# Performance work log

Hardware: AMD Instinct MI355X
Metric: run time of the kernel (lower is better)

Reference implementation:

```python
import jax, jax.numpy as jnp
import numpy as np

C = 256      # in_channels
H = 16       # num_heads
K = 7        # tconv kernel size
P1 = 8       # type_1 partition size
P2 = 8       # type_2 partition size
HB = H // 4  # heads per attention branch (= 4)
EPS = 1e-5


def _ln(x, g, b):
    m = x.mean(-1, keepdims=True)
    v = ((x - m) ** 2).mean(-1, keepdims=True)
    return (x - m) / jnp.sqrt(v + EPS) * g + b


def _window_attn(parts, table, heads, P):
    # parts: [B_, P, 3*Cb]; table: [2P-1, heads]
    B_, N, _ = parts.shape
    qkv = parts.reshape(B_, N, 3, heads, -1).transpose(2, 0, 3, 1, 4)  # [3,B_,h,P,d]
    q, k, v = qkv[0], qkv[1], qkv[2]
    scale = heads ** (-0.5)  # NOTE: module scales by num_heads**-0.5 (faithful)
    attn = jnp.einsum('bhnd,bhmd->bhnm', q * scale, k)
    idx = (jnp.arange(P)[:, None] - jnp.arange(P)[None, :]) + P - 1  # [P,P]
    bias = table[idx].transpose(2, 0, 1)  # [h,P,P]
    attn = jax.nn.softmax(attn + bias[None], axis=-1)
    out = jnp.einsum('bhnm,bhmd->bhnd', attn, v)
    return out.transpose(0, 2, 1, 3).reshape(B_, N, -1)


def _type1_part(x, P):  # x: [B,Cc,T] contiguous windows
    B, Cc, T = x.shape
    return x.reshape(B, Cc, T // P, P).transpose(0, 2, 3, 1).reshape(-1, P, Cc)


def _type1_rev(y, B, Cc, T, P):
    return y.reshape(B, T // P, P, Cc).transpose(0, 3, 1, 2).reshape(B, Cc, T)


def _type2_part(x, P):  # strided (dilated) windows
    B, Cc, T = x.shape
    return x.reshape(B, Cc, P, T // P).transpose(0, 3, 2, 1).reshape(-1, P, Cc)


def _type2_rev(y, B, Cc, T, P):
    return y.reshape(B, T // P, P, Cc).transpose(0, 3, 2, 1).reshape(B, Cc, T)


def setup_inputs() -> dict:
    key = jax.random.key(0)
    ks = jax.random.split(key, 16)
    B, T = 16, 8192
    d = {
        'x': jax.random.normal(ks[0], (B, C, T), jnp.float32),
        'g1': jnp.ones((C,), jnp.float32),
        'b1': jnp.zeros((C,), jnp.float32),
        'Wm': jax.random.normal(ks[1], (C, 2 * C), jnp.float32) * 0.02,
        'bm': jnp.zeros((2 * C,), jnp.float32),
        'Wc': jax.random.normal(ks[2], (C // 2, (C // 2) // (H // 2), K), jnp.float32) * 0.05,
        'bc': jnp.zeros((C // 2,), jnp.float32),
        'tab1': jax.random.normal(ks[3], (2 * P1 - 1, HB), jnp.float32) * 0.02,
        'tab2': jax.random.normal(ks[4], (2 * P2 - 1, HB), jnp.float32) * 0.02,
        'Wp': jax.random.normal(ks[5], (C, C), jnp.float32) * 0.02,
        'bp': jnp.zeros((C,), jnp.float32),
        'g2': jnp.ones((C,), jnp.float32),
        'b2': jnp.zeros((C,), jnp.float32),
        'W1': jax.random.normal(ks[6], (C, 4 * C), jnp.float32) * 0.02,
        'bf1': jnp.zeros((4 * C,), jnp.float32),
        'W2': jax.random.normal(ks[7], (4 * C, C), jnp.float32) * 0.02,
        'bf2': jnp.zeros((C,), jnp.float32),
    }
    return d


def _forward(x, g1, b1, Wm, bm, Wc, bc, tab1, tab2, Wp, bp, g2, b2, W1, bf1, W2, bf2):
    B, Cin, T = x.shape
    xt = x.transpose(0, 2, 1)  # [B,T,C]
    skip = xt
    f = (_ln(xt, g1, b1) @ Wm + bm).transpose(0, 2, 1)  # [B,2C,T]
    f_conv, f_attn = f[:, :Cin // 2], f[:, Cin // 2:]
    # grouped temporal conv, padding SAME
    y0 = jax.lax.conv_general_dilated(
        f_conv, Wc, window_strides=(1,), padding=[((K - 1) // 2, (K - 1) // 2)],
        feature_group_count=H // 2, dimension_numbers=('NCH', 'OIH', 'NCH')) + bc[None, :, None]
    Cb3 = 3 * Cin // 4
    fa1, fa2 = f_attn[:, :Cb3], f_attn[:, Cb3:]
    y1 = _type1_rev(_window_attn(_type1_part(fa1, P1), tab1, HB, P1), B, Cin // 4, T, P1)
    y2 = _type2_rev(_window_attn(_type2_part(fa2, P2), tab2, HB, P2), B, Cin // 4, T, P2)
    out = jnp.concatenate([y0, y1, y2], axis=1).transpose(0, 2, 1) @ Wp + bp
    out = skip + out
    h = _ln(out, g2, b2)
    h = jax.nn.gelu(h @ W1 + bf1, approximate=False) @ W2 + bf2
    out = out + h
    return out.transpose(0, 2, 1)  # [B,C,T]


def reference(x, g1, b1, Wm, bm, Wc, bc, tab1, tab2, Wp, bp, g2, b2, W1, bf1, W2, bf2):
    return _forward(x, g1, b1, Wm, bm, Wc, bc, tab1, tab2, Wp, bp, g2, b2, W1, bf1, W2, bf2)
```

## Files before the change

kernel.cpp:

```cpp
#include <hip/hip_runtime.h>
#include <hip/hip_bf16.h>

#define DI __device__ __forceinline__

typedef unsigned short u16;
typedef __attribute__((ext_vector_type(4))) float f32x4;
typedef __attribute__((ext_vector_type(8))) short short8;
typedef __attribute__((ext_vector_type(4))) short short4v;

constexpr int Bb = 16, Tt = 8192;
constexpr int M_TOT = Bb * Tt;

static DI u16 f2bf(float f) {
    union { float f; unsigned u; } v; v.f = f;
    unsigned r = v.u + 0x7fffu + ((v.u >> 16) & 1u);
    return (u16)(r >> 16);
}
static DI float bf2f(u16 u) {
    union { unsigned u; float f; } v; v.u = ((unsigned)u) << 16;
    return v.f;
}
static DI float bf2f_s(short s) { return bf2f((u16)s); }

static DI void lds_load16(const void* g, void* l) {
    __builtin_amdgcn_global_load_lds(
        (const __attribute__((address_space(1))) void*)g,
        (__attribute__((address_space(3))) void*)l, 16, 0, 0);
}

static DI float gelu_fast(float x) {
    float x2 = x * x;
    float z2 = x * (2.30220723f + 0.10294515f * x2);
    float e;
    asm("v_exp_f32 %0, %1" : "=v"(e) : "v"(z2));
    float r = __builtin_amdgcn_rcpf(1.f + e);
    return x - x * r;
}

__global__ void prep_weights(const float* __restrict__ Wm, const float* __restrict__ Wp,
                             const float* __restrict__ W1, const float* __restrict__ W2,
                             const float* __restrict__ Wc,
                             const float* __restrict__ g1, const float* __restrict__ b1,
                             const float* __restrict__ g2, const float* __restrict__ b2,
                             const float* __restrict__ bm, const float* __restrict__ bf1,
                             u16* __restrict__ WmT, u16* __restrict__ WpT,
                             u16* __restrict__ W1T, u16* __restrict__ W2T,
                             u16* __restrict__ WtC,
                             float* __restrict__ bmF, float* __restrict__ b1F) {
    int i = blockIdx.x * blockDim.x + threadIdx.x;
    int stride = gridDim.x * blockDim.x;
    for (int j = i; j < 512 * 256; j += stride) {
        int n = j >> 8, k = j & 255;
        WmT[j] = f2bf(Wm[k * 512 + n] * g1[k]);
    }
    for (int j = i; j < 256 * 256; j += stride) {
        int n = j >> 8, k = j & 255;
        WpT[j] = f2bf(Wp[k * 256 + n]);
    }
    for (int j = i; j < 1024 * 256; j += stride) {
        int n = j >> 8, k = j & 255;
        W1T[j] = f2bf(W1[k * 1024 + n] * g2[k]);
    }
    for (int j = i; j < 256 * 1024; j += stride) {
        int n = j >> 10, k = j & 1023;
        W2T[j] = f2bf(W2[k * 256 + n]);
    }
    for (int j = i; j < 128 * 128; j += stride) {
        int co = j >> 7, kp = j & 127;
        int tap = kp >> 4, ci = kp & 15;
        float v = (tap < 7) ? Wc[(co * 16 + ci) * 7 + tap] : 0.f;
        WtC[j] = f2bf(v);
    }
    for (int n = i; n < 512; n += stride) {
        float s = bm[n];
        for (int k = 0; k < 256; ++k) s += b1[k] * Wm[k * 512 + n];
        bmF[n] = s;
    }
    for (int n = i; n < 1024; n += stride) {
        float s = bf1[n];
        for (int k = 0; k < 256; ++k) s += b2[k] * W1[k * 1024 + n];
        b1F[n] = s;
    }
}

__global__ __launch_bounds__(256) void ln1_kernel(const float* __restrict__ x,
                                                  u16* __restrict__ xln,
                                                  u16* __restrict__ xt) {
    __shared__ u16 tile[64 * 256];
    __shared__ float ps[64 * 16], pss[64 * 16];
    __shared__ float smean[64], srstd[64];
    int bidx = blockIdx.x;
    int b = bidx >> 7;
    int t0 = (bidx & 127) << 6;
    int tid = threadIdx.x, l = tid & 63, w = tid >> 6;
    int lr = l & 15, lg = l >> 4;
    float s[4] = {}, ss[4] = {};
    #pragma unroll 4
    for (int it = 0; it < 16; ++it) {
        int c = it * 16 + w * 4 + lg;
        f32x4 v = *(const f32x4*)&x[((size_t)b * 256 + c) * 8192 + t0 + lr * 4];
        #pragma unroll
        for (int k = 0; k < 4; ++k) {
            s[k] += v[k]; ss[k] += v[k] * v[k];
            int t = lr * 4 + k;
            int c8 = c >> 3;
            int slot = (c8 & 24) | ((c8 ^ t) & 7);
            tile[t * 256 + slot * 8 + (c & 7)] = f2bf(v[k]);
        }
    }
    #pragma unroll
    for (int k = 0; k < 4; ++k) {
        ps[(lr * 4 + k) * 16 + w * 4 + lg] = s[k];
        pss[(lr * 4 + k) * 16 + w * 4 + lg] = ss[k];
    }
    __syncthreads();
    if (tid < 64) {
        float sum = 0.f, sq = 0.f;
        #pragma unroll
        for (int g = 0; g < 16; ++g) { sum += ps[tid * 16 + g]; sq += pss[tid * 16 + g]; }
        float m = sum * (1.f / 256.f);
        smean[tid] = m;
        srstd[tid] = rsqrtf(sq * (1.f / 256.f) - m * m + 1e-5f);
    }
    __syncthreads();
    int r = tid >> 2, q = tid & 3;
    float m = smean[r], rs = srstd[r];
    size_t rowbase = ((size_t)b * 8192 + t0 + r) * 256;
    #pragma unroll
    for (int u = 0; u < 8; ++u) {
        int c0 = q * 64 + u * 8;
        int c8 = c0 >> 3;
        int slot = (c8 & 24) | ((c8 ^ r) & 7);
        short8 d = *(const short8*)&tile[r * 256 + slot * 8];
        *(short8*)&xt[rowbase + c0] = d;
        short8 o;
        #pragma unroll
        for (int j = 0; j < 8; ++j)
            o[j] = (short)f2bf((bf2f_s(d[j]) - m) * rs);
        *(short8*)&xln[rowbase + c0] = o;
    }
}

template<int EPI, int N, int K>
__global__ __launch_bounds__(256) void gemm_bt2(const u16* __restrict__ A,
                                                const u16* __restrict__ Bt,
                                                const float* __restrict__ bias,
                                                u16* __restrict__ outb,
                                                const u16* __restrict__ skipx) {
    constexpr int NB = N / 128;
    int bid = blockIdx.x;
    int x8 = bid & 7;
    int rest = bid >> 3;
    int ni = rest % NB;
    int mi = (rest / NB) * 8 + x8;
    int m0 = mi * 128, n0 = ni * 128;
    __shared__ u16 As[2][128 * 64];
    __shared__ u16 Bs[2][128 * 64];
    int tid = threadIdx.x, l = tid & 63, w = tid >> 6;
    int mrow = (w >> 1) * 64, ncol = (w & 1) * 64;
    int lr = l & 15, lg = l >> 4;
    f32x4 acc[4][4] = {};
    auto stage = [&](int buf, int k0) {
        #pragma unroll
        for (int p = 0; p < 4; ++p) {
            int cb = p * 256 + w * 64;
            int chunk = cb + l;
            int row = chunk >> 3, k8 = chunk & 7;
            int k8s = k8 ^ (row & 7);
            lds_load16(A  + (size_t)(m0 + row) * K + k0 + k8s * 8, &As[buf][cb * 8]);
            lds_load16(Bt + (size_t)(n0 + row) * K + k0 + k8s * 8, &Bs[buf][cb * 8]);
        }
    };
    stage(0, 0);
    __syncthreads();
    constexpr int NT = K / 64;
    int buf = 0;
    for (int t = 0; t < NT; ++t) {
        if (t + 1 < NT) stage(buf ^ 1, (t + 1) * 64);
        __builtin_amdgcn_s_setprio(1);
        #pragma unroll
        for (int kk = 0; kk < 64; kk += 32) {
            short8 a[4], bfr[4];
            #pragma unroll
            for (int i = 0; i < 4; ++i) {
                int r = mrow + i * 16 + lr;
                a[i] = *(const short8*)&As[buf][r * 64 + ((((kk >> 3) + lg) ^ (r & 7)) << 3)];
            }
            #pragma unroll
            for (int j = 0; j < 4; ++j) {
                int r = ncol + j * 16 + lr;
                bfr[j] = *(const short8*)&Bs[buf][r * 64 + ((((kk >> 3) + lg) ^ (r & 7)) << 3)];
            }
            #pragma unroll
            for (int i = 0; i < 4; ++i)
                #pragma unroll
                for (int j = 0; j < 4; ++j)
                    acc[i][j] = __builtin_amdgcn_mfma_f32_16x16x32_bf16(a[i], bfr[j], acc[i][j], 0, 0, 0);
        }
        __builtin_amdgcn_s_setprio(0);
        __syncthreads();
        buf ^= 1;
    }
    #pragma unroll
    for (int i = 0; i < 4; ++i) {
        int row0 = m0 + mrow + i * 16 + lg * 4;
        #pragma unroll
        for (int j = 0; j < 4; ++j) {
            int col = n0 + ncol + j * 16 + lr;
            float bv = bias[col];
            f32x4 v = acc[i][j];
            if constexpr (EPI == 0) {
                #pragma unroll
                for (int r = 0; r < 4; ++r)
                    outb[(size_t)(row0 + r) * N + col] = f2bf(v[r] + bv);
            } else {
                #pragma unroll
                for (int r = 0; r < 4; ++r)
                    outb[(size_t)(row0 + r) * N + col] =
                        f2bf(v[r] + bv + bf2f(skipx[(size_t)(row0 + r) * 256 + col]));
            }
        }
    }
}

__global__ __launch_bounds__(1024, 1) void ffn_fused7(const u16* __restrict__ outb,
                                                      const u16* __restrict__ W1g,
                                                      const float* __restrict__ b1F,
                                                      const u16* __restrict__ W2T,
                                                      const float* __restrict__ bf2v,
                                                      float* __restrict__ out) {
    __shared__ u16 W1c[2][64 * 256];
    __shared__ u16 W2c[2][256 * 64];
    __shared__ u16 hbuf[128 * 64];
    int bid = blockIdx.x;
    int m0 = bid * 128;
    int tid = threadIdx.x, l = tid & 63, w = tid >> 6;
    int lr = l & 15, lg = l >> 4;
    int wm1 = w >> 1, wn1 = w & 1;
    int wm2 = w >> 2, wn2 = w & 3;

    short8 a_reg[8];
    {
        size_t base = (size_t)(m0 + wm1 * 16 + lr) * 256 + lg * 8;
        float s = 0.f, ss = 0.f;
        #pragma unroll
        for (int ks = 0; ks < 8; ++ks) {
            short8 rv = *(const short8*)&outb[base + ks * 32];
            a_reg[ks] = rv;
            #pragma unroll
            for (int e = 0; e < 8; ++e) { float v = bf2f_s(rv[e]); s += v; ss += v * v; }
        }
        s += __shfl_xor(s, 16); ss += __shfl_xor(ss, 16);
        s += __shfl_xor(s, 32); ss += __shfl_xor(ss, 32);
        float m = s * (1.f / 256.f);
        float rs = rsqrtf(ss * (1.f / 256.f) - m * m + 1e-5f);
        #pragma unroll
        for (int ks = 0; ks < 8; ++ks) {
            short8 rv = a_reg[ks], ov;
            #pragma unroll
            for (int e = 0; e < 8; ++e) ov[e] = (short)f2bf((bf2f_s(rv[e]) - m) * rs);
            a_reg[ks] = ov;
        }
    }

    auto stageW1 = [&](int buf, int c) {
        #pragma unroll
        for (int p = 0; p < 2; ++p) {
            int cb = p * 1024 + w * 64;
            int chunk = cb + l;
            int row = chunk >> 5, sl = chunk & 31;
            int sl2 = (sl & 24) | ((sl ^ row) & 7);
            lds_load16(W1g + (size_t)(c * 64 + row) * 256 + sl2 * 8, &W1c[buf][cb * 8]);
        }
    };
    auto stageW2 = [&](int buf, int c) {
        #pragma unroll
        for (int p = 0; p < 2; ++p) {
            int cb = p * 1024 + w * 64;
            int chunk = cb + l;
            int row = chunk >> 3, sl = chunk & 7;
            int sl2 = sl ^ (row & 7);
            lds_load16(W2T + (size_t)row * 1024 + c * 64 + sl2 * 8, &W2c[buf][cb * 8]);
        }
    };
    stageW1(0, 0); stageW2(0, 0);
    f32x4 acc2[2][4] = {};
    __syncthreads();

    for (int c = 0; c < 16; ++c) {
        int buf = c & 1;
        f32x4 acc1[2] = {};
        __builtin_amdgcn_s_setprio(1);
        #pragma unroll
        for (int ks = 0; ks < 8; ++ks) {
            short8 wf[2];
            #pragma unroll
            for (int nt = 0; nt < 2; ++nt) {
                int n = wn1 * 32 + nt * 16 + lr;
                int sl = ks * 4 + lg;
                int sl2 = (sl & 24) | ((sl ^ n) & 7);
                wf[nt] = *(const short8*)&W1c[buf][n * 256 + sl2 * 8];
            }
            #pragma unroll
            for (int nt = 0; nt < 2; ++nt)
                acc1[nt] = __builtin_amdgcn_mfma_f32_16x16x32_bf16(
                    wf[nt], a_reg[ks], acc1[nt], 0, 0, 0);
        }
        __builtin_amdgcn_s_setprio(0);
        if (c < 15) { stageW1(buf ^ 1, c + 1); stageW2(buf ^ 1, c + 1); }
        #pragma unroll
        for (int nt = 0; nt < 2; ++nt) {
            int colb = wn1 * 32 + nt * 16 + lg * 4;
            int row = wm1 * 16 + lr;
            f32x4 bv4 = *(const f32x4*)&b1F[c * 64 + colb];
            float g0 = gelu_fast(acc1[nt][0] + bv4[0]);
            float g1v = gelu_fast(acc1[nt][1] + bv4[1]);
            float g2v = gelu_fast(acc1[nt][2] + bv4[2]);
            float g3v = gelu_fast(acc1[nt][3] + bv4[3]);
            uint2 dd;
            asm("v_cvt_pk_bf16_f32 %0, %1, %2" : "=v"(dd.x) : "v"(g0), "v"(g1v));
            asm("v_cvt_pk_bf16_f32 %0, %1, %2" : "=v"(dd.y) : "v"(g2v), "v"(g3v));
            int sl2 = (colb >> 3) ^ (row & 7);
            *(uint2*)&hbuf[row * 64 + sl2 * 8 + (colb & 7)] = dd;
        }
        asm volatile("s_waitcnt lgkmcnt(0)" ::: "memory");
        __builtin_amdgcn_s_barrier();
        __builtin_amdgcn_sched_barrier(0);
        __builtin_amdgcn_s_setprio(1);
        #pragma unroll
        for (int ks = 0; ks < 2; ++ks) {
            short8 hf[2], w2f[4];
            #pragma unroll
            for (int mt = 0; mt < 2; ++mt) {
                int row = wm2 * 32 + mt * 16 + lr;
                int sl2 = (ks * 4 + lg) ^ (row & 7);
                hf[mt] = *(const short8*)&hbuf[row * 64 + sl2 * 8];
            }
            #pragma unroll
            for (int nt = 0; nt < 4; ++nt) {
                int n = wn2 * 64 + nt * 16 + lr;
                int sl2 = (ks * 4 + lg) ^ (n & 7);
                w2f[nt] = *(const short8*)&W2c[buf][n * 64 + sl2 * 8];
            }
            #pragma unroll
            for (int mt = 0; mt < 2; ++mt)
                #pragma unroll
                for (int nt = 0; nt < 4; ++nt)
                    acc2[mt][nt] = __builtin_amdgcn_mfma_f32_16x16x32_bf16(
                        hf[mt], w2f[nt], acc2[mt][nt], 0, 0, 0);
        }
        __builtin_amdgcn_s_setprio(0);
        __syncthreads();
    }
    int bb_ = m0 >> 13;
    int tb = m0 & 8191;
    #pragma unroll
    for (int mt = 0; mt < 2; ++mt) {
        int row0 = wm2 * 32 + mt * 16 + lg * 4;
        #pragma unroll
        for (int nt = 0; nt < 4; ++nt) {
            int col = wn2 * 64 + nt * 16 + lr;
            float bv = bf2v[col];
            f32x4 o;
            #pragma unroll
            for (int r = 0; r < 4; ++r)
                o[r] = acc2[mt][nt][r] + bv + bf2f(outb[(size_t)(m0 + row0 + r) * 256 + col]);
            *(f32x4*)&out[((size_t)bb_ * 256 + col) * 8192 + tb + row0] = o;
        }
    }
}

__global__ __launch_bounds__(256) void mixer_kernel(const u16* __restrict__ f,
                                                    const u16* __restrict__ WtC,
                                                    const float* __restrict__ bc,
                                                    const float* __restrict__ tab1,
                                                    const float* __restrict__ tab2,
                                                    u16* __restrict__ att) {
    __shared__ u16 smem[25600];
    __shared__ float stab[60];
    int bid = blockIdx.x;
    int path = bid % 3;
    int inner = bid / 3;
    int b = inner >> 7;
    int tid = threadIdx.x, l = tid & 63, w = tid >> 6;

    if (path == 0) {
        u16* fs = smem;
        u16* wt = smem + 9216;
        int t0 = (inner & 127) << 6;
        #pragma unroll
        for (int k = 0; k < 8; ++k) {
            int c = tid + k * 256;
            int row = c >> 4, sl = c & 15;
            int c8s = (sl & 8) | ((sl ^ row) & 7);
            lds_load16(WtC + row * 128 + c8s * 8, &wt[(w * 64 + (tid & 63)) * 8 + k * 256 * 8]);
        }
        for (int c = tid; c < 72 * 16; c += 256) {
            int rrow = c >> 4, c8 = c & 15;
            int t = t0 - 3 + rrow;
            uint4 v = {0u, 0u, 0u, 0u};
            if (t >= 0 && t < 8192)
                v = *(const uint4*)&f[((size_t)b * 8192 + t) * 512 + c8 * 8];
            int slot = (c8 & 8) | ((c8 ^ rrow) & 7);
            *(uint4*)&fs[rrow * 128 + slot * 8] = v;
        }
        __syncthreads();
        int wr = w >> 1, wc = w & 1;
        int lr = l & 15, lg = l >> 4;
        f32x4 acc[2][4] = {};
        #pragma unroll
        for (int kk = 0; kk < 4; ++kk) {
            int kp = kk * 32 + lg * 8;
            int tap = kp >> 4, ci = kp & 15;
            #pragma unroll
            for (int i = 0; i < 2; ++i) {
                int trow = wr * 32 + i * 16 + lr;
                #pragma unroll
                for (int g = 0; g < 4; ++g) {
                    int ra = trow + tap;
                    int ea = (wc * 4 + g) * 2 + (ci >> 3);
                    short8 a = *(const short8*)&fs[ra * 128 + (((ea & 8) | ((ea ^ ra) & 7)) << 3)];
                    int nb = (wc * 4 + g) * 16 + lr;
                    int eb = kp >> 3;
                    short8 bfr = *(const short8*)&wt[nb * 128 + (((eb & 8) | ((eb ^ nb) & 7)) << 3)];
                    acc[i][g] = __builtin_amdgcn_mfma_f32_16x16x32_bf16(a, bfr, acc[i][g], 0, 0, 0);
                }
            }
        }
        #pragma unroll
        for (int i = 0; i < 2; ++i) {
            int trow = wr * 32 + i * 16 + lg * 4;
            #pragma unroll
            for (int g = 0; g < 4; ++g) {
                int co = (wc * 4 + g) * 16 + lr;
                float bv = bc[co];
                #pragma unroll
                for (int r = 0; r < 4; ++r) {
                    int t = t0 + trow + r;
                    att[((size_t)b * 8192 + t) * 256 + co] = f2bf(acc[i][g][r] + bv);
                }
            }
        }
    } else {
        u16* qkv = smem;
        const int QBASE = (path == 1) ? 128 : 320;
        const int OBASE = (path == 1) ? 128 : 192;
        const float* tab = (path == 1) ? tab1 : tab2;
        int j0 = (inner & 127) << 3;
        if (tid < 60) stab[tid] = tab[tid];
        for (int c = tid; c < 64 * 24; c += 256) {
            int ridx = c / 24, off = (c % 24) << 3;
            int wl = ridx >> 3, n = ridx & 7;
            int t = (path == 1) ? ((j0 + wl) * 8 + n) : (n * 1024 + j0 + wl);
            *(uint4*)&qkv[ridx * 200 + off] = *(const uint4*)&f[((size_t)b * 8192 + t) * 512 + QBASE + off];
        }
        __syncthreads();
        int wl = tid >> 5, h = (tid >> 3) & 3, n = tid & 7;
        const u16* qr = &qkv[(wl * 8 + n) * 200 + h * 16];
        float q[16];
        {
            short8 q0 = *(const short8*)qr, q1 = *(const short8*)(qr + 8);
            #pragma unroll
            for (int d = 0; d < 8; ++d) { q[d] = bf2f_s(q0[d]); q[d + 8] = bf2f_s(q1[d]); }
        }
        float s[8];
        #pragma unroll
        for (int m = 0; m < 8; ++m) {
            const u16* kr = &qkv[(wl * 8 + m) * 200 + 64 + h * 16];
            short8 k0 = *(const short8*)kr, k1 = *(const short8*)(kr + 8);
            float a = 0.f;
            #pragma unroll
            for (int d = 0; d < 8; ++d) a += q[d] * bf2f_s(k0[d]) + q[d + 8] * bf2f_s(k1[d]);
            s[m] = 0.5f * a + stab[(n - m + 7) * 4 + h];
        }
        float mx = s[0];
        #pragma unroll
        for (int m = 1; m < 8; ++m) mx = fmaxf(mx, s[m]);
        float sum = 0.f;
        #pragma unroll
        for (int m = 0; m < 8; ++m) { s[m] = __expf(s[m] - mx); sum += s[m]; }
        float rinv = 1.f / sum;
        float o[16] = {};
        #pragma unroll
        for (int m = 0; m < 8; ++m) {
            float p = s[m] * rinv;
            const u16* vr = &qkv[(wl * 8 + m) * 200 + 128 + h * 16];
            short8 v0 = *(const short8*)vr, v1 = *(const short8*)(vr + 8);
            #pragma unroll
            for (int d = 0; d < 8; ++d) { o[d] += p * bf2f_s(v0[d]); o[d + 8] += p * bf2f_s(v1[d]); }
        }
        int t = (path == 1) ? ((j0 + wl) * 8 + n) : (n * 1024 + j0 + wl);
        short8 o0, o1;
        #pragma unroll
        for (int d = 0; d < 8; ++d) { o0[d] = (short)f2bf(o[d]); o1[d] = (short)f2bf(o[d + 8]); }
        u16* op = &att[((size_t)b * 8192 + t) * 256 + OBASE + h * 16];
        *(short8*)op = o0; *(short8*)(op + 8) = o1;
    }
}

extern "C" void kernel_launch(void* const* d_in, const int* in_sizes, int n_in,
                              void* d_out, int out_size, void* d_ws, size_t ws_size,
                              hipStream_t stream) {
    const float* x    = (const float*)d_in[0];
    const float* g1   = (const float*)d_in[1];
    const float* b1   = (const float*)d_in[2];
    const float* Wm   = (const float*)d_in[3];
    const float* bm   = (const float*)d_in[4];
    const float* Wc   = (const float*)d_in[5];
    const float* bc   = (const float*)d_in[6];
    const float* tab1 = (const float*)d_in[7];
    const float* tab2 = (const float*)d_in[8];
    const float* Wp   = (const float*)d_in[9];
    const float* bp   = (const float*)d_in[10];
    const float* g2   = (const float*)d_in[11];
    const float* b2   = (const float*)d_in[12];
    const float* W1   = (const float*)d_in[13];
    const float* bf1  = (const float*)d_in[14];
    const float* W2   = (const float*)d_in[15];
    const float* bf2  = (const float*)d_in[16];
    float* out = (float*)d_out;

    char* ws = (char*)d_ws;
    u16* f    = (u16*)(ws);
    u16* att  = (u16*)(ws + 134217728);
    u16* outb = (u16*)(ws + 201326592);
    u16* xlnb = (u16*)(ws + 268435456);
    u16* xt   = (u16*)(ws + 335544320);
    char* wb = ws + 402653184;
    u16* WmT   = (u16*)wb;
    u16* WpT   = (u16*)(wb + 262144);
    u16* W1T   = (u16*)(wb + 393216);
    u16* W2T   = (u16*)(wb + 917504);
    u16* WtC   = (u16*)(wb + 1441792);
    float* bmF = (float*)(wb + 1474560);
    float* b1F = (float*)(wb + 1476608);

    prep_weights<<<512, 256, 0, stream>>>(Wm, Wp, W1, W2, Wc, g1, b1, g2, b2, bm, bf1,
                                          WmT, WpT, W1T, W2T, WtC, bmF, b1F);
    ln1_kernel<<<Bb * (Tt / 64), 256, 0, stream>>>(x, xlnb, xt);
    gemm_bt2<0, 512, 256><<<(M_TOT / 128) * 4, 256, 0, stream>>>(xlnb, WmT, bmF, f, nullptr);
    mixer_kernel<<<3 * Bb * 128, 256, 0, stream>>>(f, WtC, bc, tab1, tab2, att);
    gemm_bt2<1, 256, 256><<<(M_TOT / 128) * 2, 256, 0, stream>>>(att, WpT, bp, outb, xt);
    ffn_fused7<<<M_TOT / 128, 1024, 0, stream>>>(outb, W1T, b1F, W2T, bf2, out);
}
```

Measured before the change: 492.8 us.

## Fold LayerNorm normalization into GEMM epilogue via mean/rstd and weight column sums

LN1 no longer writes a normalized bf16 copy of the activations. It stores per-row mean and rstd, and the first GEMM consumes the raw bf16 transpose directly. The epilogue applies rstd*(acc - mean*colsum(g1*Wm)) + bias, where the column sums are precomputed in prep_weights. This removes one full 64 MB bf16 write and its dependent pass, at the cost of some precision, because centering now happens after the bf16 GEMM, which risks cancellation.

```diff
diff --git a/kernel.cpp b/kernel.cpp
--- a/kernel.cpp
+++ b/kernel.cpp
@@ -46,7 +46,8 @@
                              u16* __restrict__ WmT, u16* __restrict__ WpT,
                              u16* __restrict__ W1T, u16* __restrict__ W2T,
                              u16* __restrict__ WtC,
-                             float* __restrict__ bmF, float* __restrict__ b1F) {
+                             float* __restrict__ bmF, float* __restrict__ b1F,
+                             float* __restrict__ colsum) {
     int i = blockIdx.x * blockDim.x + threadIdx.x;
     int stride = gridDim.x * blockDim.x;
     for (int j = i; j < 512 * 256; j += stride) {
@@ -72,9 +73,13 @@
         WtC[j] = f2bf(v);
     }
     for (int n = i; n < 512; n += stride) {
-        float s = bm[n];
-        for (int k = 0; k < 256; ++k) s += b1[k] * Wm[k * 512 + n];
+        float s = bm[n], cs = 0.f;
+        for (int k = 0; k < 256; ++k) {
+            s += b1[k] * Wm[k * 512 + n];
+            cs += g1[k] * Wm[k * 512 + n];
+        }
         bmF[n] = s;
+        colsum[n] = cs;
     }
     for (int n = i; n < 1024; n += stride) {
         float s = bf1[n];
@@ -84,11 +89,11 @@
 }
 
 __global__ __launch_bounds__(256) void ln1_kernel(const float* __restrict__ x,
-                                                  u16* __restrict__ xln,
-                                                  u16* __restrict__ xt) {
+                                                  u16* __restrict__ xt,
+                                                  float* __restrict__ mbuf,
+                                                  float* __restrict__ rbuf) {
     __shared__ u16 tile[64 * 256];
     __shared__ float ps[64 * 16], pss[64 * 16];
-    __shared__ float smean[64], srstd[64];
     int bidx = blockIdx.x;
     int b = bidx >> 7;
     int t0 = (bidx & 127) << 6;
@@ -119,12 +124,10 @@
         #pragma unroll
         for (int g = 0; g < 16; ++g) { sum += ps[tid * 16 + g]; sq += pss[tid * 16 + g]; }
         float m = sum * (1.f / 256.f);
-        smean[tid] = m;
-        srstd[tid] = rsqrtf(sq * (1.f / 256.f) - m * m + 1e-5f);
-    }
-    __syncthreads();
+        mbuf[(size_t)b * 8192 + t0 + tid] = m;
+        rbuf[(size_t)b * 8192 + t0 + tid] = rsqrtf(sq * (1.f / 256.f) - m * m + 1e-5f);
+    }
     int r = tid >> 2, q = tid & 3;
-    float m = smean[r], rs = srstd[r];
     size_t rowbase = ((size_t)b * 8192 + t0 + r) * 256;
     #pragma unroll
     for (int u = 0; u < 8; ++u) {
@@ -133,11 +136,6 @@
         int slot = (c8 & 24) | ((c8 ^ r) & 7);
         short8 d = *(const short8*)&tile[r * 256 + slot * 8];
         *(short8*)&xt[rowbase + c0] = d;
-        short8 o;
-        #pragma unroll
-        for (int j = 0; j < 8; ++j)
-            o[j] = (short)f2bf((bf2f_s(d[j]) - m) * rs);
-        *(short8*)&xln[rowbase + c0] = o;
     }
 }
 
@@ -146,7 +144,10 @@
                                                 const u16* __restrict__ Bt,
                                                 const float* __restrict__ bias,
                                                 u16* __restrict__ outb,
-                                                const u16* __restrict__ skipx) {
+                                                const u16* __restrict__ skipx,
+                                                const float* __restrict__ mbuf,
+                                                const float* __restrict__ rbuf,
+                                                const float* __restrict__ colsum) {
     constexpr int NB = N / 128;
     int bid = blockIdx.x;
     int x8 = bid & 7;
@@ -204,15 +205,22 @@
     #pragma unroll
     for (int i = 0; i < 4; ++i) {
         int row0 = m0 + mrow + i * 16 + lg * 4;
+        f32x4 mv, rv;
+        if constexpr (EPI == 0) {
+            mv = *(const f32x4*)&mbuf[row0];
+            rv = *(const f32x4*)&rbuf[row0];
+        }
         #pragma unroll
         for (int j = 0; j < 4; ++j) {
             int col = n0 + ncol + j * 16 + lr;
             float bv = bias[col];
             f32x4 v = acc[i][j];
             if constexpr (EPI == 0) {
+                float cs = colsum[col];
                 #pragma unroll
                 for (int r = 0; r < 4; ++r)
-                    outb[(size_t)(row0 + r) * N + col] = f2bf(v[r] + bv);
+                    outb[(size_t)(row0 + r) * N + col] =
+                        f2bf(rv[r] * (v[r] - mv[r] * cs) + bv);
             } else {
                 #pragma unroll
                 for (int r = 0; r < 4; ++r)
@@ -524,22 +532,26 @@
     u16* f    = (u16*)(ws);
     u16* att  = (u16*)(ws + 134217728);
     u16* outb = (u16*)(ws + 201326592);
-    u16* xlnb = (u16*)(ws + 268435456);
     u16* xt   = (u16*)(ws + 335544320);
     char* wb = ws + 402653184;
-    u16* WmT   = (u16*)wb;
-    u16* WpT   = (u16*)(wb + 262144);
-    u16* W1T   = (u16*)(wb + 393216);
-    u16* W2T   = (u16*)(wb + 917504);
-    u16* WtC   = (u16*)(wb + 1441792);
-    float* bmF = (float*)(wb + 1474560);
-    float* b1F = (float*)(wb + 1476608);
+    u16* WmT    = (u16*)wb;
+    u16* WpT    = (u16*)(wb + 262144);
+    u16* W1T    = (u16*)(wb + 393216);
+    u16* W2T    = (u16*)(wb + 917504);
+    u16* WtC    = (u16*)(wb + 1441792);
+    float* bmF  = (float*)(wb + 1474560);
+    float* b1F  = (float*)(wb + 1476608);
+    float* cs1  = (float*)(wb + 1480704);
+    float* mbuf = (float*)(wb + 1482752);
+    float* rbuf = (float*)(wb + 2007040);
 
     prep_weights<<<512, 256, 0, stream>>>(Wm, Wp, W1, W2, Wc, g1, b1, g2, b2, bm, bf1,
-                                          WmT, WpT, W1T, W2T, WtC, bmF, b1F);
-    ln1_kernel<<<Bb * (Tt / 64), 256, 0, stream>>>(x, xlnb, xt);
-    gemm_bt2<0, 512, 256><<<(M_TOT / 128) * 4, 256, 0, stream>>>(xlnb, WmT, bmF, f, nullptr);
+                                          WmT, WpT, W1T, W2T, WtC, bmF, b1F, cs1);
+    ln1_kernel<<<Bb * (Tt / 64), 256, 0, stream>>>(x, xt, mbuf, rbuf);
+    gemm_bt2<0, 512, 256><<<(M_TOT / 128) * 4, 256, 0, stream>>>(xt, WmT, bmF, f, nullptr,
+                                                                 mbuf, rbuf, cs1);
     mixer_kernel<<<3 * Bb * 128, 256, 0, stream>>>(f, WtC, bc, tab1, tab2, att);
-    gemm_bt2<1, 256, 256><<<(M_TOT / 128) * 2, 256, 0, stream>>>(att, WpT, bp, outb, xt);
+    gemm_bt2<1, 256, 256><<<(M_TOT / 128) * 2, 256, 0, stream>>>(att, WpT, bp, outb, xt,
+                                                                 nullptr, nullptr, nullptr);
     ffn_fused7<<<M_TOT / 128, 1024, 0, stream>>>(outb, W1T, b1F, W2T, bf2, out);
 }
```

After: 462.5 us. 1.07x faster.
